# Kernel tuning notes

Measured on AMD Instinct MI355X. Metric: run time of the kernel, lower is better.

The kernel has to match this reference:

```python
import jax, jax.numpy as jnp
import numpy as np

B, N, E = 1024, 81, 1620
H, M, NSTEPS = 128, 128, 8


def setup_inputs() -> dict:
    key = jax.random.key(0)
    ks = jax.random.split(key, 16)
    s = lambda i, shape, fan: jax.random.normal(ks[i], shape, jnp.float32) * (1.0 / np.sqrt(fan))
    return {
        "x": jax.random.normal(ks[0], (B, N, 10), jnp.float32),
        "edge_index": jax.random.randint(ks[1], (2, E), 0, N, jnp.int64),
        # input_proj: Linear(10, H)
        "W_in": s(2, (H, 10), 10), "b_in": jnp.zeros((H,), jnp.float32),
        # msg_mlp: Linear(2H, M) -> ReLU -> Linear(M, M)
        "W_m1": s(3, (M, 2 * H), 2 * H), "b_m1": jnp.zeros((M,), jnp.float32),
        "W_m2": s(4, (M, M), M), "b_m2": jnp.zeros((M,), jnp.float32),
        # GRUCell(M, H): weights stacked [r; z; n]
        "W_ih": s(5, (3 * H, M), M), "W_hh": s(6, (3 * H, H), H),
        "b_ih": jnp.zeros((3 * H,), jnp.float32), "b_hh": jnp.zeros((3 * H,), jnp.float32),
        # output_head: Dropout (eval=no-op) -> Linear(H, H) -> ReLU -> Linear(H, 9)
        "W_o1": s(7, (H, H), H), "b_o1": jnp.zeros((H,), jnp.float32),
        "W_o2": s(8, (9, H), H), "b_o2": jnp.zeros((9,), jnp.float32),
    }


def reference(x, edge_index, W_in, b_in, W_m1, b_m1, W_m2, b_m2,
              W_ih, W_hh, b_ih, b_hh, W_o1, b_o1, W_o2, b_o2):
    senders, receivers = edge_index[0], edge_index[1]
    h = x @ W_in.T + b_in                       # (B, N, H)
    for _ in range(NSTEPS):
        h_send = h[:, senders, :]               # (B, E, H) gather
        h_recv = h[:, receivers, :]             # (B, E, H) gather
        msg_in = jnp.concatenate([h_send, h_recv], axis=-1)   # (B, E, 2H)
        msgs = jax.nn.relu(msg_in @ W_m1.T + b_m1) @ W_m2.T + b_m2  # (B, E, M)
        agg = jnp.zeros((h.shape[0], N, M), msgs.dtype).at[:, receivers, :].add(msgs)
        # GRUCell: gates ordered [r, z, n] as in torch
        gi = agg @ W_ih.T + b_ih                # (B, N, 3H)
        gh = h @ W_hh.T + b_hh                  # (B, N, 3H)
        r = jax.nn.sigmoid(gi[..., :H] + gh[..., :H])
        z = jax.nn.sigmoid(gi[..., H:2 * H] + gh[..., H:2 * H])
        n = jnp.tanh(gi[..., 2 * H:] + r * gh[..., 2 * H:])
        h = (1.0 - z) * n + z * h
    hid = jax.nn.relu(h @ W_o1.T + b_o1)        # dropout is identity in eval
    return hid @ W_o2.T + b_o2                  # (B, N, 9)
```

## Files before the change

### kernel.cpp

```cpp
#include <hip/hip_runtime.h>

#define BB 1024
#define NN 81
#define EE 1620
#define HH 128
#define G3 384
#define NSTEPS 8

#define HSTR 132
#define ABSTR 260

typedef __attribute__((ext_vector_type(4))) float f32x4;

#define F_H     0
#define F_R2    10692
#define F_GOFF  31752
#define F_GSEND 31834
#define F_BM1   32644
#define F_BASE  32772
#define F_EXT   33284
#define F_TOT   33796
#define LDS_BYTES (F_TOT * 4)

__global__ __launch_bounds__(128) void prep_graph(const int* __restrict__ ei,
                                                  int* __restrict__ goff,
                                                  int* __restrict__ gsend) {
    __shared__ int eis[2 * EE];
    __shared__ int cs[NN];
    __shared__ int offs[NN + 1];
    int tid = threadIdx.x;
    for (int i = tid; i < 2 * EE; i += 128) eis[i] = ei[i];
    __syncthreads();
    if (tid < NN) {
        int c = 0;
        for (int e = 0; e < EE; e++) if (eis[EE + e] == tid) c++;
        cs[tid] = c;
    }
    __syncthreads();
    if (tid == 0) {
        int o = 0;
        for (int r = 0; r < NN; r++) { offs[r] = o; o += cs[r]; }
        offs[NN] = o;
    }
    __syncthreads();
    if (tid < NN) {
        int pos = offs[tid];
        for (int e = 0; e < EE; e++) {
            if (eis[EE + e] == tid) gsend[pos++] = eis[e];
        }
        goff[tid] = offs[tid];
    }
    if (tid == 0) goff[NN] = offs[NN];
}

__global__ __launch_bounds__(256) void prep_wc(const float* __restrict__ W_ih,
                                               const float* __restrict__ W_m2,
                                               float* __restrict__ Wc) {
    int idx = blockIdx.x * 256 + threadIdx.x;
    if (idx >= G3 * HH) return;
    int c = idx >> 7, o = idx & 127;
    float acc = 0.f;
    for (int m = 0; m < HH; m++) acc += W_ih[c * HH + m] * W_m2[m * HH + o];
    Wc[idx] = acc;
}

__global__ __launch_bounds__(256) void prep_bias(const float* __restrict__ W_ih,
                                                 const float* __restrict__ b_m2,
                                                 const float* __restrict__ b_ih,
                                                 const float* __restrict__ b_hh,
                                                 float* __restrict__ basev,
                                                 float* __restrict__ extv) {
    int c = blockIdx.x * 256 + threadIdx.x;
    if (c >= 512) return;
    float base, ext;
    if (c < 384) {
        float bwc = 0.f;
        for (int m = 0; m < HH; m++) bwc += W_ih[c * HH + m] * b_m2[m];
        ext = bwc;
        base = (c < 256) ? (b_ih[c] + b_hh[c]) : b_ih[c];
    } else {
        ext = 0.f;
        base = b_hh[c - 128];
    }
    basev[c] = base;
    extv[c] = ext;
}

__global__ __launch_bounds__(256) void prep_w1q(const float* __restrict__ W_m1,
                                                float* __restrict__ W1q) {
    int idx = blockIdx.x * 256 + threadIdx.x;
    if (idx >= 128 * 256) return;
    int k = idx >> 8, c = idx & 255;
    float v = (c < 128) ? W_m1[c * 256 + k] : W_m1[(c - 128) * 256 + 128 + k];
    W1q[((k >> 2) * 256 + c) * 4 + (k & 3)] = v;
}

__global__ __launch_bounds__(256) void prep_wgq(const float* __restrict__ Wc,
                                                const float* __restrict__ W_hh,
                                                float* __restrict__ Wgq) {
    int idx = blockIdx.x * 256 + threadIdx.x;
    if (idx >= 256 * G3) return;
    int k = idx / G3;
    int c = idx - k * G3;
    float v = (k < 128) ? Wc[c * HH + k] : W_hh[c * HH + (k - 128)];
    Wgq[((k >> 2) * G3 + c) * 4 + (k & 3)] = v;
}

__global__ __launch_bounds__(256) void prep_wo1q(const float* __restrict__ W_o1,
                                                 float* __restrict__ Wo1q) {
    int idx = blockIdx.x * 256 + threadIdx.x;
    if (idx >= 128 * 128) return;
    int k = idx >> 7, c = idx & 127;
    Wo1q[((k >> 2) * 128 + c) * 4 + (k & 3)] = W_o1[c * HH + k];
}

__global__ __launch_bounds__(512, 2) void fused_rrn(
    const float* __restrict__ x,
    const float* __restrict__ W_in, const float* __restrict__ b_in,
    const float* __restrict__ b_m1,
    const float* __restrict__ W1q, const float* __restrict__ Wgq,
    const float* __restrict__ basev, const float* __restrict__ extv,
    const float* __restrict__ Wo1q, const float* __restrict__ b_o1,
    const float* __restrict__ W_o2, const float* __restrict__ b_o2,
    const int* __restrict__ goff_g, const int* __restrict__ gsend_g,
    float* __restrict__ out)
{
    extern __shared__ float smf[];
    float* hRM  = smf + F_H;
    float* reg2 = smf + F_R2;
    int*   goffL = (int*)(smf + F_GOFF);
    unsigned short* gsendL = (unsigned short*)(smf + F_GSEND);
    float* bm1L  = smf + F_BM1;
    float* baseL = smf + F_BASE;
    float* extL  = smf + F_EXT;

    const int t   = threadIdx.x;
    const int b   = blockIdx.x;
    const int c32 = t & 31;
    const int g   = t >> 5;
    const int rowBase = g * 5;
    const int nR = (g == 15) ? 6 : 5;
    const int rW = t & 31;
    const int f8 = 8 * (t >> 5);

    float* xsL  = reg2;
    float* winL = reg2 + 810;
    for (int i = t; i < NN + 1; i += 512) goffL[i] = goff_g[i];
    for (int i = t; i < EE; i += 512) gsendL[i] = (unsigned short)gsend_g[i];
    baseL[t] = basev[t];
    extL[t]  = extv[t];
    if (t < 128) bm1L[t] = b_m1[t];
    for (int i = t; i < NN * 10; i += 512) xsL[i] = x[(long)b * (NN * 10) + i];
    for (int i = t; i < HH * 10; i += 512) winL[i] = W_in[i];
    __syncthreads();

    for (int idx = t; idx < NN * HH; idx += 512) {
        int r = idx >> 7, m = idx & 127;
        float acc = b_in[m];
#pragma unroll
        for (int k = 0; k < 10; k++) acc += xsL[r * 10 + k] * winL[m * 10 + k];
        hRM[r * HSTR + m] = acc;
    }
    __syncthreads();

    for (int step = 0; step < NSTEPS; step++) {
        {
            float accA[6][4], accB[6][4];
#pragma unroll
            for (int i = 0; i < 6; i++)
#pragma unroll
                for (int j = 0; j < 4; j++) { accA[i][j] = 0.f; accB[i][j] = 0.f; }
            for (int kc = 0; kc < 128; kc += 4) {
                const int q4 = kc >> 2;
                f32x4 bA[4], bB[4];
#pragma unroll
                for (int j = 0; j < 4; j++) {
                    bA[j] = *(const f32x4*)(W1q + (q4 * 256 + c32 + 32 * j) * 4);
                    bB[j] = *(const f32x4*)(W1q + (q4 * 256 + 128 + c32 + 32 * j) * 4);
                }
#pragma unroll
                for (int i = 0; i < 6; i++) {
                    if (i < nR) {
                        f32x4 a = *(const f32x4*)(hRM + (rowBase + i) * HSTR + kc);
#pragma unroll
                        for (int j = 0; j < 4; j++)
#pragma unroll
                            for (int kk = 0; kk < 4; kk++) {
                                accA[i][j] = fmaf(a[kk], bA[j][kk], accA[i][j]);
                                accB[i][j] = fmaf(a[kk], bB[j][kk], accB[i][j]);
                            }
                    }
                }
            }
            float* hAB = reg2;
#pragma unroll
            for (int i = 0; i < 6; i++) {
                if (i < nR) {
                    int row = rowBase + i;
#pragma unroll
                    for (int j = 0; j < 4; j++) {
                        hAB[row * ABSTR + c32 + 32 * j] = accA[i][j];
                        hAB[row * ABSTR + 128 + c32 + 32 * j] = accB[i][j];
                    }
                }
            }
        }
        __syncthreads();

        float sv[3][8];
        {
            float bq[8];
#pragma unroll
            for (int j = 0; j < 8; j++) bq[j] = bm1L[f8 + j];
#pragma unroll
            for (int s = 0; s < 3; s++) {
                int row = rW + 32 * s;
                if (row >= NN) {
#pragma unroll
                    for (int j = 0; j < 8; j++) sv[s][j] = 0.f;
                    continue;
                }
                int e0 = goffL[row], e1 = goffL[row + 1];
                f32x4 hb0 = *(const f32x4*)(reg2 + row * ABSTR + 128 + f8);
                f32x4 hb1 = *(const f32x4*)(reg2 + row * ABSTR + 128 + f8 + 4);
                float hbb[8], ac[8];
#pragma unroll
                for (int j = 0; j < 4; j++) {
                    hbb[j] = hb0[j] + bq[j];
                    hbb[4 + j] = hb1[j] + bq[4 + j];
                    ac[j] = 0.f; ac[4 + j] = 0.f;
                }
                for (int e = e0; e < e1; e++) {
                    int sn = gsendL[e];
                    f32x4 av0 = *(const f32x4*)(reg2 + sn * ABSTR + f8);
                    f32x4 av1 = *(const f32x4*)(reg2 + sn * ABSTR + f8 + 4);
#pragma unroll
                    for (int j = 0; j < 4; j++) {
                        ac[j]     += fmaxf(av0[j] + hbb[j], 0.f);
                        ac[4 + j] += fmaxf(av1[j] + hbb[4 + j], 0.f);
                    }
                }
#pragma unroll
                for (int j = 0; j < 8; j++) sv[s][j] = ac[j];
            }
        }
        __syncthreads();
        {
#pragma unroll
            for (int s = 0; s < 3; s++) {
                int row = rW + 32 * s;
                if (row >= NN) continue;
                f32x4 v0 = {sv[s][0], sv[s][1], sv[s][2], sv[s][3]};
                f32x4 v1 = {sv[s][4], sv[s][5], sv[s][6], sv[s][7]};
                *(f32x4*)(reg2 + row * HSTR + f8) = v0;
                *(f32x4*)(reg2 + row * HSTR + f8 + 4) = v1;
            }
        }
        __syncthreads();

        {
            const float* smRM = reg2;
            float rg_[6][4], z[6][4];
            {
                float rr[6][4], zz[6][4];
#pragma unroll
                for (int i = 0; i < 6; i++)
#pragma unroll
                    for (int j = 0; j < 4; j++) { rr[i][j] = 0.f; zz[i][j] = 0.f; }
                for (int kc = 0; kc < 128; kc += 4) {
                    const int g4 = kc >> 2;
                    f32x4 bR[4], bZ[4];
#pragma unroll
                    for (int j = 0; j < 4; j++) {
                        bR[j] = *(const f32x4*)(Wgq + (g4 * G3 + c32 + 32 * j) * 4);
                        bZ[j] = *(const f32x4*)(Wgq + (g4 * G3 + 128 + c32 + 32 * j) * 4);
                    }
#pragma unroll
                    for (int i = 0; i < 6; i++) {
                        if (i < nR) {
                            f32x4 a = *(const f32x4*)(smRM + (rowBase + i) * HSTR + kc);
#pragma unroll
                            for (int j = 0; j < 4; j++)
#pragma unroll
                                for (int kk = 0; kk < 4; kk++) {
                                    rr[i][j] = fmaf(a[kk], bR[j][kk], rr[i][j]);
                                    zz[i][j] = fmaf(a[kk], bZ[j][kk], zz[i][j]);
                                }
                        }
                    }
                }
                for (int kc = 0; kc < 128; kc += 4) {
                    const int g4 = (128 + kc) >> 2;
                    f32x4 bR[4], bZ[4];
#pragma unroll
                    for (int j = 0; j < 4; j++) {
                        bR[j] = *(const f32x4*)(Wgq + (g4 * G3 + c32 + 32 * j) * 4);
                        bZ[j] = *(const f32x4*)(Wgq + (g4 * G3 + 128 + c32 + 32 * j) * 4);
                    }
#pragma unroll
                    for (int i = 0; i < 6; i++) {
                        if (i < nR) {
                            f32x4 a = *(const f32x4*)(hRM + (rowBase + i) * HSTR + kc);
#pragma unroll
                            for (int j = 0; j < 4; j++)
#pragma unroll
                                for (int kk = 0; kk < 4; kk++) {
                                    rr[i][j] = fmaf(a[kk], bR[j][kk], rr[i][j]);
                                    zz[i][j] = fmaf(a[kk], bZ[j][kk], zz[i][j]);
                                }
                        }
                    }
                }
#pragma unroll
                for (int i = 0; i < 6; i++) {
                    if (i < nR) {
                        int row = rowBase + i;
                        float cf = (float)(goffL[row + 1] - goffL[row]);
#pragma unroll
                        for (int j = 0; j < 4; j++) {
                            int cc = c32 + 32 * j;
                            float g0 = rr[i][j] + baseL[cc] + cf * extL[cc];
                            float g1 = zz[i][j] + baseL[128 + cc] + cf * extL[128 + cc];
                            rg_[i][j] = 1.f / (1.f + __expf(-g0));
                            z[i][j]   = 1.f / (1.f + __expf(-g1));
                        }
                    }
                }
            }
            float tmp[6][4];
            {
                float nh[6][4];
#pragma unroll
                for (int i = 0; i < 6; i++)
#pragma unroll
                    for (int j = 0; j < 4; j++) nh[i][j] = 0.f;
                for (int kc = 0; kc < 128; kc += 4) {
                    const int g4 = (128 + kc) >> 2;
                    f32x4 bN[4];
#pragma unroll
                    for (int j = 0; j < 4; j++)
                        bN[j] = *(const f32x4*)(Wgq + (g4 * G3 + 256 + c32 + 32 * j) * 4);
#pragma unroll
                    for (int i = 0; i < 6; i++) {
                        if (i < nR) {
                            f32x4 a = *(const f32x4*)(hRM + (rowBase + i) * HSTR + kc);
#pragma unroll
                            for (int j = 0; j < 4; j++)
#pragma unroll
                                for (int kk = 0; kk < 4; kk++)
                                    nh[i][j] = fmaf(a[kk], bN[j][kk], nh[i][j]);
                        }
                    }
                }
#pragma unroll
                for (int i = 0; i < 6; i++) {
                    if (i < nR) {
#pragma unroll
                        for (int j = 0; j < 4; j++)
                            tmp[i][j] = rg_[i][j] * (nh[i][j] + baseL[384 + c32 + 32 * j]);
                    }
                }
            }
            {
                float ni[6][4];
#pragma unroll
                for (int i = 0; i < 6; i++)
#pragma unroll
                    for (int j = 0; j < 4; j++) ni[i][j] = 0.f;
                for (int kc = 0; kc < 128; kc += 4) {
                    const int g4 = kc >> 2;
                    f32x4 bN[4];
#pragma unroll
                    for (int j = 0; j < 4; j++)
                        bN[j] = *(const f32x4*)(Wgq + (g4 * G3 + 256 + c32 + 32 * j) * 4);
#pragma unroll
                    for (int i = 0; i < 6; i++) {
                        if (i < nR) {
                            f32x4 a = *(const f32x4*)(smRM + (rowBase + i) * HSTR + kc);
#pragma unroll
                            for (int j = 0; j < 4; j++)
#pragma unroll
                                for (int kk = 0; kk < 4; kk++)
                                    ni[i][j] = fmaf(a[kk], bN[j][kk], ni[i][j]);
                        }
                    }
                }
                __syncthreads();

#pragma unroll
                for (int i = 0; i < 6; i++) {
                    if (i < nR) {
                        int row = rowBase + i;
                        float cf = (float)(goffL[row + 1] - goffL[row]);
#pragma unroll
                        for (int j = 0; j < 4; j++) {
                            int cc = c32 + 32 * j;
                            float npre = ni[i][j] + baseL[256 + cc] + cf * extL[256 + cc] + tmp[i][j];
                            float ax = fabsf(npre);
                            float e  = __expf(-2.f * ax);
                            float tt = (1.f - e) / (1.f + e);
                            float n  = copysignf(tt, npre);
                            float ho = hRM[row * HSTR + cc];
                            hRM[row * HSTR + cc] = (1.f - z[i][j]) * n + z[i][j] * ho;
                        }
                    }
                }
            }
        }
        __syncthreads();
    }

    {
        float acc3[6][4];
#pragma unroll
        for (int i = 0; i < 6; i++)
#pragma unroll
            for (int j = 0; j < 4; j++) acc3[i][j] = 0.f;
        for (int kc = 0; kc < 128; kc += 4) {
            f32x4 bb[4];
#pragma unroll
            for (int j = 0; j < 4; j++)
                bb[j] = *(const f32x4*)(Wo1q + ((kc >> 2) * 128 + c32 + 32 * j) * 4);
#pragma unroll
            for (int i = 0; i < 6; i++) {
                if (i < nR) {
                    f32x4 a = *(const f32x4*)(hRM + (rowBase + i) * HSTR + kc);
#pragma unroll
                    for (int j = 0; j < 4; j++)
#pragma unroll
                        for (int kk = 0; kk < 4; kk++)
                            acc3[i][j] = fmaf(a[kk], bb[j][kk], acc3[i][j]);
                }
            }
        }
        __syncthreads();
#pragma unroll
        for (int i = 0; i < 6; i++) {
            if (i < nR) {
                int row = rowBase + i;
#pragma unroll
                for (int j = 0; j < 4; j++) {
                    int cc = c32 + 32 * j;
                    reg2[row * HSTR + cc] = fmaxf(acc3[i][j] + b_o1[cc], 0.f);
                }
            }
        }
    }
    __syncthreads();
    {
        float* wo2L = hRM;
        float* bo2L = hRM + 1152;
        for (int i = t; i < 9 * HH; i += 512) wo2L[i] = W_o2[i];
        if (t < 9) bo2L[t] = b_o2[t];
    }
    __syncthreads();
    {
        const float* wo2L = hRM;
        const float* bo2L = hRM + 1152;
        for (int idx = t; idx < NN * 9; idx += 512) {
            int r = idx / 9, qq = idx - 9 * r;
            float acc = bo2L[qq];
            const float* hrow = reg2 + r * HSTR;
            const float* wrow = wo2L + qq * HH;
            for (int k = 0; k < HH; k++) acc = fmaf(hrow[k], wrow[k], acc);
            out[((long)b * NN + r) * 9 + qq] = acc;
        }
    }
}

extern "C" void kernel_launch(void* const* d_in, const int* in_sizes, int n_in,
                              void* d_out, int out_size, void* d_ws, size_t ws_size,
                              hipStream_t stream) {
    const float* x      = (const float*)d_in[0];
    const int* ei       = (const int*)d_in[1];
    const float* W_in   = (const float*)d_in[2];
    const float* b_in   = (const float*)d_in[3];
    const float* W_m1   = (const float*)d_in[4];
    const float* b_m1   = (const float*)d_in[5];
    const float* W_m2   = (const float*)d_in[6];
    const float* b_m2   = (const float*)d_in[7];
    const float* W_ih   = (const float*)d_in[8];
    const float* W_hh   = (const float*)d_in[9];
    const float* b_ih   = (const float*)d_in[10];
    const float* b_hh   = (const float*)d_in[11];
    const float* W_o1   = (const float*)d_in[12];
    const float* b_o1   = (const float*)d_in[13];
    const float* W_o2   = (const float*)d_in[14];
    const float* b_o2   = (const float*)d_in[15];
    float* out = (float*)d_out;

    char* ws = (char*)d_ws;
    size_t off = 0;
    auto alloc = [&](size_t bytes) -> char* {
        char* p = ws + off;
        off += (bytes + 255) & ~(size_t)255;
        return p;
    };
    float* Wc    = (float*)alloc((size_t)G3 * HH * 4);
    float* W1q   = (float*)alloc(128 * 256 * 4);
    float* Wgq   = (float*)alloc(256 * G3 * 4);
    float* Wo1q  = (float*)alloc(128 * 128 * 4);
    float* basev = (float*)alloc(512 * 4);
    float* extv  = (float*)alloc(512 * 4);
    int* goff    = (int*)alloc((NN + 1) * 4);
    int* gsend   = (int*)alloc(EE * 4);

    prep_graph<<<1, 128, 0, stream>>>(ei, goff, gsend);
    prep_wc<<<(G3 * HH + 255) / 256, 256, 0, stream>>>(W_ih, W_m2, Wc);
    prep_bias<<<2, 256, 0, stream>>>(W_ih, b_m2, b_ih, b_hh, basev, extv);
    prep_w1q<<<128, 256, 0, stream>>>(W_m1, W1q);
    prep_wgq<<<(256 * G3 + 255) / 256, 256, 0, stream>>>(Wc, W_hh, Wgq);
    prep_wo1q<<<64, 256, 0, stream>>>(W_o1, Wo1q);

    (void)hipFuncSetAttribute((const void*)fused_rrn,
                              hipFuncAttributeMaxDynamicSharedMemorySize,
                              (int)LDS_BYTES);
    fused_rrn<<<BB, 512, LDS_BYTES, stream>>>(
        x, W_in, b_in, b_m1, W1q, Wgq, basev, extv,
        Wo1q, b_o1, W_o2, b_o2, goff, gsend, out);
}
```

Before: 3.425 ms.

## Stage weight tiles in LDS with double-buffered register prefetch for GEMMs

Result: slower. 4.891 ms (+42.8%).

```diff
diff --git a/kernel.cpp b/kernel.cpp
--- a/kernel.cpp
+++ b/kernel.cpp
@@ -19,7 +19,8 @@
 #define F_BM1   32644
 #define F_BASE  32772
 #define F_EXT   33284
-#define F_TOT   33796
+#define F_BST   33796
+#define F_TOT   37892
 #define LDS_BYTES (F_TOT * 4)
 
 __global__ __launch_bounds__(128) void prep_graph(const int* __restrict__ ei,
@@ -133,6 +134,7 @@
     float* bm1L  = smf + F_BM1;
     float* baseL = smf + F_BASE;
     float* extL  = smf + F_EXT;
+    float* Bst   = smf + F_BST;
 
     const int t   = threadIdx.x;
     const int b   = blockIdx.x;
@@ -142,6 +144,8 @@
     const int nR = (g == 15) ? 6 : 5;
     const int rW = t & 31;
     const int f8 = 8 * (t >> 5);
+    const int sq = t >> 8, scol = t & 255;
+    const int q2 = t >> 7, col2 = t & 127;
 
     float* xsL  = reg2;
     float* winL = reg2 + 810;
@@ -170,27 +174,44 @@
             for (int i = 0; i < 6; i++)
 #pragma unroll
                 for (int j = 0; j < 4; j++) { accA[i][j] = 0.f; accB[i][j] = 0.f; }
-            for (int kc = 0; kc < 128; kc += 4) {
-                const int q4 = kc >> 2;
-                f32x4 bA[4], bB[4];
-#pragma unroll
-                for (int j = 0; j < 4; j++) {
-                    bA[j] = *(const f32x4*)(W1q + (q4 * 256 + c32 + 32 * j) * 4);
-                    bB[j] = *(const f32x4*)(W1q + (q4 * 256 + 128 + c32 + 32 * j) * 4);
-                }
-#pragma unroll
-                for (int i = 0; i < 6; i++) {
-                    if (i < nR) {
-                        f32x4 a = *(const f32x4*)(hRM + (rowBase + i) * HSTR + kc);
-#pragma unroll
-                        for (int j = 0; j < 4; j++)
-#pragma unroll
-                            for (int kk = 0; kk < 4; kk++) {
-                                accA[i][j] = fmaf(a[kk], bA[j][kk], accA[i][j]);
-                                accB[i][j] = fmaf(a[kk], bB[j][kk], accB[i][j]);
-                            }
-                    }
-                }
+
+            f32x4 pf;
+            {
+                f32x4 v0 = *(const f32x4*)(W1q + (sq * 256 + scol) * 4);
+                *(f32x4*)(Bst + t * 4) = v0;
+                pf = *(const f32x4*)(W1q + ((2 + sq) * 256 + scol) * 4);
+            }
+            __syncthreads();
+            for (int ch = 0; ch < 16; ch++) {
+                const int cur = ch & 1;
+                if (ch + 1 < 16) *(f32x4*)(Bst + (cur ^ 1) * 2048 + t * 4) = pf;
+                if (ch + 2 < 16) pf = *(const f32x4*)(W1q + ((2 * (ch + 2) + sq) * 256 + scol) * 4);
+                __syncthreads();
+                const float* Bb = Bst + cur * 2048;
+#pragma unroll
+                for (int kl = 0; kl < 2; kl++) {
+                    const int kc = ch * 8 + kl * 4;
+                    f32x4 bA[4], bB[4];
+#pragma unroll
+                    for (int j = 0; j < 4; j++) {
+                        bA[j] = *(const f32x4*)(Bb + (kl * 256 + c32 + 32 * j) * 4);
+                        bB[j] = *(const f32x4*)(Bb + (kl * 256 + 128 + c32 + 32 * j) * 4);
+                    }
+#pragma unroll
+                    for (int i = 0; i < 6; i++) {
+                        if (i < nR) {
+                            f32x4 a = *(const f32x4*)(hRM + (rowBase + i) * HSTR + kc);
+#pragma unroll
+                            for (int j = 0; j < 4; j++)
+#pragma unroll
+                                for (int kk = 0; kk < 4; kk++) {
+                                    accA[i][j] = fmaf(a[kk], bA[j][kk], accA[i][j]);
+                                    accB[i][j] = fmaf(a[kk], bB[j][kk], accB[i][j]);
+                                }
+                        }
+                    }
+                }
+                __syncthreads();
             }
             float* hAB = reg2;
 #pragma unroll
@@ -267,49 +288,46 @@
                 for (int i = 0; i < 6; i++)
 #pragma unroll
                     for (int j = 0; j < 4; j++) { rr[i][j] = 0.f; zz[i][j] = 0.f; }
-                for (int kc = 0; kc < 128; kc += 4) {
-                    const int g4 = kc >> 2;
-                    f32x4 bR[4], bZ[4];
-#pragma unroll
-                    for (int j = 0; j < 4; j++) {
-                        bR[j] = *(const f32x4*)(Wgq + (g4 * G3 + c32 + 32 * j) * 4);
-                        bZ[j] = *(const f32x4*)(Wgq + (g4 * G3 + 128 + c32 + 32 * j) * 4);
-                    }
-#pragma unroll
-                    for (int i = 0; i < 6; i++) {
-                        if (i < nR) {
-                            f32x4 a = *(const f32x4*)(smRM + (rowBase + i) * HSTR + kc);
-#pragma unroll
-                            for (int j = 0; j < 4; j++)
-#pragma unroll
-                                for (int kk = 0; kk < 4; kk++) {
-                                    rr[i][j] = fmaf(a[kk], bR[j][kk], rr[i][j]);
-                                    zz[i][j] = fmaf(a[kk], bZ[j][kk], zz[i][j]);
-                                }
-                        }
-                    }
-                }
-                for (int kc = 0; kc < 128; kc += 4) {
-                    const int g4 = (128 + kc) >> 2;
-                    f32x4 bR[4], bZ[4];
-#pragma unroll
-                    for (int j = 0; j < 4; j++) {
-                        bR[j] = *(const f32x4*)(Wgq + (g4 * G3 + c32 + 32 * j) * 4);
-                        bZ[j] = *(const f32x4*)(Wgq + (g4 * G3 + 128 + c32 + 32 * j) * 4);
-                    }
-#pragma unroll
-                    for (int i = 0; i < 6; i++) {
-                        if (i < nR) {
-                            f32x4 a = *(const f32x4*)(hRM + (rowBase + i) * HSTR + kc);
-#pragma unroll
-                            for (int j = 0; j < 4; j++)
-#pragma unroll
-                                for (int kk = 0; kk < 4; kk++) {
-                                    rr[i][j] = fmaf(a[kk], bR[j][kk], rr[i][j]);
-                                    zz[i][j] = fmaf(a[kk], bZ[j][kk], zz[i][j]);
-                                }
-                        }
-                    }
+
+                f32x4 pf;
+                {
+                    f32x4 v0 = *(const f32x4*)(Wgq + (sq * G3 + scol) * 4);
+                    *(f32x4*)(Bst + t * 4) = v0;
+                    pf = *(const f32x4*)(Wgq + ((2 + sq) * G3 + scol) * 4);
+                }
+                __syncthreads();
+                for (int ch = 0; ch < 32; ch++) {
+                    const int cur = ch & 1;
+                    if (ch + 1 < 32) *(f32x4*)(Bst + (cur ^ 1) * 2048 + t * 4) = pf;
+                    if (ch + 2 < 32) pf = *(const f32x4*)(Wgq + ((2 * (ch + 2) + sq) * G3 + scol) * 4);
+                    __syncthreads();
+                    const float* Bb = Bst + cur * 2048;
+                    const float* Ab = (ch < 16) ? smRM : hRM;
+                    const int kcb = (ch & 15) * 8;
+#pragma unroll
+                    for (int kl = 0; kl < 2; kl++) {
+                        const int kc = kcb + kl * 4;
+                        f32x4 bR[4], bZ[4];
+#pragma unroll
+                        for (int j = 0; j < 4; j++) {
+                            bR[j] = *(const f32x4*)(Bb + (kl * 256 + c32 + 32 * j) * 4);
+                            bZ[j] = *(const f32x4*)(Bb + (kl * 256 + 128 + c32 + 32 * j) * 4);
+                        }
+#pragma unroll
+                        for (int i = 0; i < 6; i++) {
+                            if (i < nR) {
+                                f32x4 a = *(const f32x4*)(Ab + (rowBase + i) * HSTR + kc);
+#pragma unroll
+                                for (int j = 0; j < 4; j++)
+#pragma unroll
+                                    for (int kk = 0; kk < 4; kk++) {
+                                        rr[i][j] = fmaf(a[kk], bR[j][kk], rr[i][j]);
+                                        zz[i][j] = fmaf(a[kk], bZ[j][kk], zz[i][j]);
+                                    }
+                            }
+                        }
+                    }
+                    __syncthreads();
                 }
 #pragma unroll
                 for (int i = 0; i < 6; i++) {
@@ -334,23 +352,42 @@
                 for (int i = 0; i < 6; i++)
 #pragma unroll
                     for (int j = 0; j < 4; j++) nh[i][j] = 0.f;
-                for (int kc = 0; kc < 128; kc += 4) {
-                    const int g4 = (128 + kc) >> 2;
-                    f32x4 bN[4];
-#pragma unroll
-                    for (int j = 0; j < 4; j++)
-                        bN[j] = *(const f32x4*)(Wgq + (g4 * G3 + 256 + c32 + 32 * j) * 4);
-#pragma unroll
-                    for (int i = 0; i < 6; i++) {
-                        if (i < nR) {
-                            f32x4 a = *(const f32x4*)(hRM + (rowBase + i) * HSTR + kc);
-#pragma unroll
-                            for (int j = 0; j < 4; j++)
-#pragma unroll
-                                for (int kk = 0; kk < 4; kk++)
-                                    nh[i][j] = fmaf(a[kk], bN[j][kk], nh[i][j]);
-                        }
-                    }
+
+                f32x4 pf;
+                if (t < 256) {
+                    f32x4 v0 = *(const f32x4*)(Wgq + ((32 + q2) * G3 + 256 + col2) * 4);
+                    *(f32x4*)(Bst + t * 4) = v0;
+                    pf = *(const f32x4*)(Wgq + ((34 + q2) * G3 + 256 + col2) * 4);
+                }
+                __syncthreads();
+                for (int ch = 0; ch < 16; ch++) {
+                    const int cur = ch & 1;
+                    if (t < 256) {
+                        if (ch + 1 < 16) *(f32x4*)(Bst + (cur ^ 1) * 2048 + t * 4) = pf;
+                        if (ch + 2 < 16) pf = *(const f32x4*)(Wgq + ((32 + 2 * (ch + 2) + q2) * G3 + 256 + col2) * 4);
+                    }
+                    __syncthreads();
+                    const float* Bb = Bst + cur * 2048;
+#pragma unroll
+                    for (int kl = 0; kl < 2; kl++) {
+                        const int kc = ch * 8 + kl * 4;
+                        f32x4 bN[4];
+#pragma unroll
+                        for (int j = 0; j < 4; j++)
+                            bN[j] = *(const f32x4*)(Bb + (kl * 128 + c32 + 32 * j) * 4);
+#pragma unroll
+                        for (int i = 0; i < 6; i++) {
+                            if (i < nR) {
+                                f32x4 a = *(const f32x4*)(hRM + (rowBase + i) * HSTR + kc);
+#pragma unroll
+                                for (int j = 0; j < 4; j++)
+#pragma unroll
+                                    for (int kk = 0; kk < 4; kk++)
+                                        nh[i][j] = fmaf(a[kk], bN[j][kk], nh[i][j]);
+                            }
+                        }
+                    }
+                    __syncthreads();
                 }
 #pragma unroll
                 for (int i = 0; i < 6; i++) {
@@ -367,26 +404,43 @@
                 for (int i = 0; i < 6; i++)
 #pragma unroll
                     for (int j = 0; j < 4; j++) ni[i][j] = 0.f;
-                for (int kc = 0; kc < 128; kc += 4) {
-                    const int g4 = kc >> 2;
-                    f32x4 bN[4];
-#pragma unroll
-                    for (int j = 0; j < 4; j++)
-                        bN[j] = *(const f32x4*)(Wgq + (g4 * G3 + 256 + c32 + 32 * j) * 4);
-#pragma unroll
-                    for (int i = 0; i < 6; i++) {
-                        if (i < nR) {
-                            f32x4 a = *(const f32x4*)(smRM + (rowBase + i) * HSTR + kc);
-#pragma unroll
-                            for (int j = 0; j < 4; j++)
-#pragma unroll
-                                for (int kk = 0; kk < 4; kk++)
-                                    ni[i][j] = fmaf(a[kk], bN[j][kk], ni[i][j]);
-                        }
-                    }
+
+                f32x4 pf;
+                if (t < 256) {
+                    f32x4 v0 = *(const f32x4*)(Wgq + (q2 * G3 + 256 + col2) * 4);
+                    *(f32x4*)(Bst + t * 4) = v0;
+                    pf = *(const f32x4*)(Wgq + ((2 + q2) * G3 + 256 + col2) * 4);
                 }
                 __syncthreads();
-
+                for (int ch = 0; ch < 16; ch++) {
+                    const int cur = ch & 1;
+                    if (t < 256) {
+                        if (ch + 1 < 16) *(f32x4*)(Bst + (cur ^ 1) * 2048 + t * 4) = pf;
+                        if (ch + 2 < 16) pf = *(const f32x4*)(Wgq + ((2 * (ch + 2) + q2) * G3 + 256 + col2) * 4);
+                    }
+                    __syncthreads();
+                    const float* Bb = Bst + cur * 2048;
+#pragma unroll
+                    for (int kl = 0; kl < 2; kl++) {
+                        const int kc = ch * 8 + kl * 4;
+                        f32x4 bN[4];
+#pragma unroll
+                        for (int j = 0; j < 4; j++)
+                            bN[j] = *(const f32x4*)(Bb + (kl * 128 + c32 + 32 * j) * 4);
+#pragma unroll
+                        for (int i = 0; i < 6; i++) {
+                            if (i < nR) {
+                                f32x4 a = *(const f32x4*)(smRM + (rowBase + i) * HSTR + kc);
+#pragma unroll
+                                for (int j = 0; j < 4; j++)
+#pragma unroll
+                                    for (int kk = 0; kk < 4; kk++)
+                                        ni[i][j] = fmaf(a[kk], bN[j][kk], ni[i][j]);
+                            }
+                        }
+                    }
+                    __syncthreads();
+                }
 #pragma unroll
                 for (int i = 0; i < 6; i++) {
                     if (i < nR) {
```
